# Optimization experiments

Measured on AMD Instinct MI355X. Metric: run time of the kernel, lower is better.

## Reference

```python
import jax, jax.numpy as jnp
import numpy as np

# ---- static IOBES label set: 'O' + {B,I,E,S}-T{t} for 12 entity types -> 49 labels ----
N_TYPES = 12
LABEL_NAMES = ['O'] + [f'{p}-T{t}' for t in range(N_TYPES) for p in ('B', 'I', 'E', 'S')]
L = len(LABEL_NAMES)  # 49

def _build_allow():
    # ALLOW[prev, nxt] True iff transition prev->nxt is NOT masked by mask_logits
    A = np.zeros((L, L), dtype=bool)
    for i, pname in enumerate(LABEL_NAMES):
        if pname[0] in 'OES':
            for j, nname in enumerate(LABEL_NAMES):
                A[i, j] = nname[0] in 'OBS'
        else:  # B-tag or I-tag: only I-tag / E-tag allowed
            tag = pname.split('-')[-1]
            for j, nname in enumerate(LABEL_NAMES):
                A[i, j] = nname in (f'I-{tag}', f'E-{tag}')
    return A

ALLOW = jnp.asarray(_build_allow())
NEG = -1e12

B, S, H, E = 64, 512, 1024, 128


def setup_inputs() -> dict:
    key = jax.random.key(0)
    ks = jax.random.split(key, 8)
    scale = 0.02
    return {
        'word_embeddings': jax.random.normal(ks[0], (B, S, H), dtype=jnp.float32),
        'label_ids': jax.random.randint(ks[1], (B, S), 0, L, dtype=jnp.int32),
        'emb_table': jax.random.normal(ks[2], (L, E), dtype=jnp.float32) * scale,
        'w_ih': jax.random.normal(ks[3], (3 * H, E + H), dtype=jnp.float32) * scale,
        'w_hh': jax.random.normal(ks[4], (3 * H, H), dtype=jnp.float32) * scale,
        'b_ih': jnp.zeros((3 * H,), dtype=jnp.float32),
        'b_hh': jnp.zeros((3 * H,), dtype=jnp.float32),
        'w_out': jax.random.normal(ks[5], (L, H), dtype=jnp.float32) * scale,
        'b_out': jnp.zeros((L,), dtype=jnp.float32),
    }


def reference(word_embeddings, label_ids, emb_table, w_ih, w_hh, b_ih, b_hh, w_out, b_out):
    Bn, Sn, Hn = word_embeddings.shape
    # teacher-forced previous labels, shifted right with 'O' (index 0) start token
    start = jnp.zeros((Bn, 1), dtype=label_ids.dtype)
    prev_ids = jnp.concatenate([start, label_ids], axis=1)[:, :-1]  # [B,S]
    # per-step GRU input: [prev label embedding ; word embedding]
    x = jnp.concatenate([emb_table[prev_ids], word_embeddings], axis=-1)  # [B,S,E+H]
    # precompute input contributions to all 3 gates for every step
    gx = jnp.einsum('bsi,gi->bsg', x, w_ih) + b_ih  # [B,S,3H], gate order r,z,n (torch)
    h0 = jnp.zeros((Bn, Hn), dtype=word_embeddings.dtype)

    def step(h, gxt):
        gh = h @ w_hh.T + b_hh  # [B,3H]
        r = jax.nn.sigmoid(gxt[:, :Hn] + gh[:, :Hn])
        z = jax.nn.sigmoid(gxt[:, Hn:2 * Hn] + gh[:, Hn:2 * Hn])
        n = jnp.tanh(gxt[:, 2 * Hn:] + r * gh[:, 2 * Hn:])
        h_new = (1.0 - z) * n + z * h
        return h_new, h_new

    _, outs = jax.lax.scan(step, h0, jnp.swapaxes(gx, 0, 1))  # [S,B,H]
    outs = jnp.swapaxes(outs, 0, 1)  # [B,S,H]
    logits = outs @ w_out.T + b_out  # [B,S,L]
    # label-transition masking based on previous label id (static IOBES constraint)
    logits = jnp.where(ALLOW[prev_ids], logits, NEG)
    return logits
```

## Files before the change

### kernel.cpp

```cpp
#include <hip/hip_runtime.h>
#include <cstdint>
#include <cstddef>

#define B_ 64
#define S_ 512
#define H_ 1024
#define E_ 128
#define L_ 49
#define G3_ 3072
#define K_ 1152
#define C_ 64
#define NCH_ 8

typedef short bf16x8 __attribute__((ext_vector_type(8)));
typedef float f32x4 __attribute__((ext_vector_type(4)));
typedef unsigned int u32x2 __attribute__((ext_vector_type(2)));

__device__ __forceinline__ unsigned short f2bf(float f) {
  unsigned int u = __builtin_bit_cast(unsigned int, f);
  return (unsigned short)((u + 0x7FFFu + ((u >> 16) & 1u)) >> 16);
}
__device__ __forceinline__ float bf2f(unsigned short h) {
  unsigned int u = ((unsigned int)h) << 16;
  return __builtin_bit_cast(float, u);
}

#define GLOAD16(dst, a64) asm volatile("global_load_dwordx4 %0, %1, off sc0 sc1" : "=v"(dst) : "v"(a64))
#define GLOAD8(dst, a64)  asm volatile("global_load_dwordx2 %0, %1, off sc0 sc1" : "=v"(dst) : "v"(a64))
#define GSTORE8(a64, v2)  asm volatile("global_store_dwordx2 %0, %1, off sc0 sc1" :: "v"(a64), "v"(v2) : "memory")
#define WAITV(N) asm volatile("s_waitcnt vmcnt(" #N ")")

__global__ __launch_bounds__(256) void init_kernel(float4* __restrict__ p)
{
  const int i = blockIdx.x * 256 + threadIdx.x;
  p[i] = make_float4(0.f, 0.f, 0.f, 0.f);
}

__global__ __launch_bounds__(256) void gx_gemm(
    const float* __restrict__ word, const int* __restrict__ labels,
    const float* __restrict__ emb, const float* __restrict__ w_ih,
    const float* __restrict__ b_ih, float* __restrict__ gxC, int t0)
{
  __shared__ float xs[2][32][72];
  __shared__ float wsm[2][32][136];

  const int bid = blockIdx.x;
  const int Tl = bid / 24;
  const int T  = t0 + Tl;
  const int cb = bid % 24;
  const int tid = threadIdx.x;

  const int xb = tid >> 2, xkq = tid & 3;
  const int pid = (T > 0) ? labels[xb * S_ + T - 1] : 0;
  const float* xsrcA = emb + (size_t)pid * E_;
  const float* xsrcB = word + ((size_t)xb * S_ + T) * H_ - E_;
  const int wc = tid >> 1, wkh = tid & 1;
  const float* wrow = w_ih + (size_t)(cb * 128 + wc) * K_;

  float4 xr0, xr1, wr0, wr1, wr2, wr3;

  auto load_tile = [&](int kt) {
    const int kg = kt * 32;
    const float* xsrc = (kg < E_) ? (xsrcA + kg) : (xsrcB + kg);
    xr0 = *(const float4*)(xsrc + xkq * 8);
    xr1 = *(const float4*)(xsrc + xkq * 8 + 4);
    const float* wsrc = wrow + kg + wkh * 16;
    wr0 = *(const float4*)(wsrc);
    wr1 = *(const float4*)(wsrc + 4);
    wr2 = *(const float4*)(wsrc + 8);
    wr3 = *(const float4*)(wsrc + 12);
  };
  auto store_tile = [&](int bf) {
#pragma unroll
    for (int i = 0; i < 4; ++i) xs[bf][xkq * 8 + i][xb]     = ((const float*)&xr0)[i];
#pragma unroll
    for (int i = 0; i < 4; ++i) xs[bf][xkq * 8 + 4 + i][xb] = ((const float*)&xr1)[i];
#pragma unroll
    for (int i = 0; i < 4; ++i) wsm[bf][wkh * 16 + i][wc]      = ((const float*)&wr0)[i];
#pragma unroll
    for (int i = 0; i < 4; ++i) wsm[bf][wkh * 16 + 4 + i][wc]  = ((const float*)&wr1)[i];
#pragma unroll
    for (int i = 0; i < 4; ++i) wsm[bf][wkh * 16 + 8 + i][wc]  = ((const float*)&wr2)[i];
#pragma unroll
    for (int i = 0; i < 4; ++i) wsm[bf][wkh * 16 + 12 + i][wc] = ((const float*)&wr3)[i];
  };

  const int cg = tid >> 4, bg = tid & 15;
  float acc[8][4];
#pragma unroll
  for (int i = 0; i < 8; ++i)
#pragma unroll
    for (int j = 0; j < 4; ++j) acc[i][j] = 0.f;

  load_tile(0);
  store_tile(0);
  __syncthreads();

  for (int kt = 0; kt < 36; ++kt) {
    const int cur = kt & 1;
    if (kt < 35) load_tile(kt + 1);
#pragma unroll 4
    for (int k = 0; k < 32; ++k) {
      const float4 xv  = *(const float4*)&xs[cur][k][bg * 4];
      const float4 wv0 = *(const float4*)&wsm[cur][k][cg * 8];
      const float4 wv1 = *(const float4*)&wsm[cur][k][cg * 8 + 4];
      const float wv[8] = {wv0.x, wv0.y, wv0.z, wv0.w, wv1.x, wv1.y, wv1.z, wv1.w};
      const float xa[4] = {xv.x, xv.y, xv.z, xv.w};
#pragma unroll
      for (int ci = 0; ci < 8; ++ci)
#pragma unroll
        for (int bi = 0; bi < 4; ++bi)
          acc[ci][bi] = fmaf(wv[ci], xa[bi], acc[ci][bi]);
    }
    if (kt < 35) store_tile(cur ^ 1);
    __syncthreads();
  }

  const size_t obase = ((size_t)Tl * G3_ + (size_t)cb * 128) * 64;
#pragma unroll
  for (int ci = 0; ci < 8; ++ci) {
    const int c = cg * 8 + ci;
    const float bv = b_ih[cb * 128 + c];
    float4 o;
    o.x = acc[ci][0] + bv; o.y = acc[ci][1] + bv;
    o.z = acc[ci][2] + bv; o.w = acc[ci][3] + bv;
    *(float4*)&gxC[obase + (size_t)c * 64 + bg * 4] = o;
  }
}

__global__ __launch_bounds__(256, 1) void scan_kernel(
    const float* __restrict__ gxC, const float* __restrict__ w_hh,
    const float* __restrict__ b_hh,
    char* phiA, char* ploA, char* phiB, char* ploB,
    float* __restrict__ outsC, unsigned* bar, unsigned step0)
{
  const int g = blockIdx.x;
  const int tid = threadIdx.x;
  const int lane = tid & 63;
  const int w = tid >> 6;
  const int m = lane & 15;
  const int gA = lane >> 4;
  const int bl = m;

  bf16x8 whi[32], wlo[32];
  {
    const bool valid = (m < 12);
    const int msafe = valid ? m : 0;
    const float* wr = w_hh + (size_t)((msafe >> 2) * 1024 + 4 * g + (msafe & 3)) * 1024;
#pragma unroll
    for (int ks = 0; ks < 32; ++ks) {
      const int kb = ks * 32 + gA * 8;
      float v[8];
      const float4 a0 = *(const float4*)(wr + kb);
      const float4 a1 = *(const float4*)(wr + kb + 4);
      v[0] = a0.x; v[1] = a0.y; v[2] = a0.z; v[3] = a0.w;
      v[4] = a1.x; v[5] = a1.y; v[6] = a1.z; v[7] = a1.w;
#pragma unroll
      for (int i = 0; i < 8; ++i) {
        const float f = valid ? v[i] : 0.f;
        const unsigned short hh = f2bf(f);
        const unsigned short hl = f2bf(f - bf2f(hh));
        whi[ks][i] = (short)hh;
        wlo[ks][i] = (short)hl;
      }
    }
  }

  const int ksj = g >> 3;
  const int gf  = (g >> 1) & 3;
  const unsigned gbyte =
      ((unsigned)((ksj * 4 + w) * 64 + gf * 16 + bl)) * 16u + 8u * (g & 1);
  float bh_r[4], bh_z[4], bh_n[4], hold[4];
#pragma unroll
  for (int jj = 0; jj < 4; ++jj) {
    bh_r[jj] = b_hh[4 * g + jj];
    bh_z[jj] = b_hh[1024 + 4 * g + jj];
    bh_n[jj] = b_hh[2048 + 4 * g + jj];
  }
  {
    u32x2 dh, dl;
    GLOAD8(dh, (uint64_t)(uintptr_t)(phiA + gbyte));
    GLOAD8(dl, (uint64_t)(uintptr_t)(ploA + gbyte));
    WAITV(0);
    __builtin_amdgcn_sched_barrier(0);
#pragma unroll
    for (int jj = 0; jj < 4; ++jj) {
      const unsigned short hh = (unsigned short)((dh[jj >> 1] >> ((jj & 1) * 16)) & 0xFFFFu);
      const unsigned short hl = (unsigned short)((dl[jj >> 1] >> ((jj & 1) * 16)) & 0xFFFFu);
      hold[jj] = bf2f(hh) + bf2f(hl);
    }
  }

  char* curHi = phiA; char* curLo = ploA;
  char* nxtHi = phiB; char* nxtLo = ploB;

  for (int s = 0; s < C_; ++s) {
    float gr[4], gz[4], gn[4];
    {
      const float* gp = gxC + (size_t)s * (G3_ * 64) + 16 * w + bl;
#pragma unroll
      for (int jj = 0; jj < 4; ++jj) {
        gr[jj] = gp[(0 * 1024 + 4 * g + jj) * 64];
        gz[jj] = gp[(1 * 1024 + 4 * g + jj) * 64];
        gn[jj] = gp[(2 * 1024 + 4 * g + jj) * 64];
      }
    }

    const uint64_t bHi = (uint64_t)(uintptr_t)curHi + (unsigned)((w << 10) + (lane << 4));
    const uint64_t bLo = (uint64_t)(uintptr_t)curLo + (unsigned)((w << 10) + (lane << 4));
    bf16x8 bh[2][4], blo[2][4];
    f32x4 acc[6];
#pragma unroll
    for (int c = 0; c < 6; ++c) acc[c] = (f32x4){0.f, 0.f, 0.f, 0.f};

#pragma unroll
    for (int q = 0; q < 4; ++q) {
      GLOAD16(bh[0][q],  bHi + (unsigned)((0 * 4 + q) * 4096));
      GLOAD16(blo[0][q], bLo + (unsigned)((0 * 4 + q) * 4096));
    }
#pragma unroll
    for (int q = 0; q < 4; ++q) {
      GLOAD16(bh[1][q],  bHi + (unsigned)((1 * 4 + q) * 4096));
      GLOAD16(blo[1][q], bLo + (unsigned)((1 * 4 + q) * 4096));
    }

#pragma unroll
    for (int grp = 0; grp < 8; ++grp) {
      if (grp < 7) { WAITV(8); } else { WAITV(0); }
      __builtin_amdgcn_sched_barrier(0);
      const int buf = grp & 1;
#pragma unroll
      for (int q = 0; q < 4; ++q) {
        const int ks = grp * 4 + q;
        const int p = (ks & 1) * 3;
        acc[p + 0] = __builtin_amdgcn_mfma_f32_16x16x32_bf16(whi[ks], bh[buf][q],  acc[p + 0], 0, 0, 0);
        acc[p + 1] = __builtin_amdgcn_mfma_f32_16x16x32_bf16(whi[ks], blo[buf][q], acc[p + 1], 0, 0, 0);
        acc[p + 2] = __builtin_amdgcn_mfma_f32_16x16x32_bf16(wlo[ks], bh[buf][q],  acc[p + 2], 0, 0, 0);
      }
      if (grp + 2 < 8) {
#pragma unroll
        for (int q = 0; q < 4; ++q) {
          GLOAD16(bh[buf][q],  bHi + (unsigned)(((grp + 2) * 4 + q) * 4096));
          GLOAD16(blo[buf][q], bLo + (unsigned)(((grp + 2) * 4 + q) * 4096));
        }
      }
    }

    f32x4 P = (acc[0] + acc[3]) + (acc[1] + acc[4]) + (acc[2] + acc[5]);

    float zs[4], ns[4];
#pragma unroll
    for (int jj = 0; jj < 4; ++jj) {
      zs[jj] = __shfl(P[jj], bl + 16);
      ns[jj] = __shfl(P[jj], bl + 32);
    }

    if (lane < 16) {
      const int b = 16 * w + bl;
      unsigned short hhi[4], hlo[4];
#pragma unroll
      for (int jj = 0; jj < 4; ++jj) {
        const float r = 1.f / (1.f + expf(-(gr[jj] + P[jj] + bh_r[jj])));
        const float z = 1.f / (1.f + expf(-(gz[jj] + zs[jj] + bh_z[jj])));
        const float n = tanhf(gn[jj] + r * (ns[jj] + bh_n[jj]));
        const float hnew = (1.f - z) * n + z * hold[jj];
        hold[jj] = hnew;
        outsC[((size_t)s << 16) + (size_t)((4 * g + jj) << 6) + b] = hnew;
        hhi[jj] = f2bf(hnew);
        hlo[jj] = f2bf(hnew - bf2f(hhi[jj]));
      }
      u32x2 vh, vl;
      vh[0] = (unsigned)hhi[0] | ((unsigned)hhi[1] << 16);
      vh[1] = (unsigned)hhi[2] | ((unsigned)hhi[3] << 16);
      vl[0] = (unsigned)hlo[0] | ((unsigned)hlo[1] << 16);
      vl[1] = (unsigned)hlo[2] | ((unsigned)hlo[3] << 16);
      GSTORE8((uint64_t)(uintptr_t)(nxtHi + gbyte), vh);
      GSTORE8((uint64_t)(uintptr_t)(nxtLo + gbyte), vl);
    }

    __syncthreads();
    if (tid == 0) {
      asm volatile("s_waitcnt vmcnt(0)" ::: "memory");
      const unsigned tgt = step0 + (unsigned)s + 1u;
      const unsigned old =
          __hip_atomic_fetch_add(bar, 1u, __ATOMIC_RELAXED, __HIP_MEMORY_SCOPE_AGENT);
      if (old == 255u) {
        __hip_atomic_store(bar, 0u, __ATOMIC_RELAXED, __HIP_MEMORY_SCOPE_AGENT);
        asm volatile("s_waitcnt vmcnt(0)" ::: "memory");
        __hip_atomic_store(bar + 544, tgt, __ATOMIC_RELAXED, __HIP_MEMORY_SCOPE_AGENT);
      } else {
        while (__hip_atomic_load(bar + 544, __ATOMIC_RELAXED, __HIP_MEMORY_SCOPE_AGENT) < tgt)
          __builtin_amdgcn_s_sleep(1);
      }
    }
    __syncthreads();

    char* t1 = curHi; curHi = nxtHi; nxtHi = t1;
    char* t2 = curLo; curLo = nxtLo; nxtLo = t2;
  }
}

__global__ __launch_bounds__(256) void logits_kernel(
    const float* __restrict__ outsC, const int* __restrict__ labels,
    const float* __restrict__ w_out, const float* __restrict__ b_out,
    float* __restrict__ out, int t0)
{
  __shared__ float hs[128 * 64];
  __shared__ float wso[49 * 128];
  const int tl = blockIdx.x;
  const int t  = t0 + tl;
  const int tid = threadIdx.x;
  const int b = tid & 63, lq = tid >> 6;
  const int l0 = lq * 13;
  const int nl = (lq == 3) ? 10 : 13;

  float acc[13];
#pragma unroll
  for (int i = 0; i < 13; ++i) acc[i] = 0.f;

  for (int kc = 0; kc < 8; ++kc) {
    __syncthreads();
#pragma unroll
    for (int i = 0; i < 8; ++i) {
      const int flat = (i << 10) + (tid << 2);
      *(float4*)&hs[flat] = *(const float4*)&outsC[((size_t)tl << 16) + (kc << 13) + flat];
    }
    for (int idx = tid; idx < 1568; idx += 256) {
      const int l = idx >> 5, k4 = idx & 31;
      *(float4*)&wso[l * 128 + (k4 << 2)] =
          *(const float4*)&w_out[(size_t)l * 1024 + (kc << 7) + (k4 << 2)];
    }
    __syncthreads();
    for (int k = 0; k < 128; k += 4) {
      const float h0 = hs[((k + 0) << 6) + b];
      const float h1 = hs[((k + 1) << 6) + b];
      const float h2 = hs[((k + 2) << 6) + b];
      const float h3 = hs[((k + 3) << 6) + b];
#pragma unroll
      for (int li = 0; li < 13; ++li) {
        if (li < nl) {
          const float4 wv = *(const float4*)&wso[(l0 + li) * 128 + k];
          acc[li] = fmaf(wv.w, h3, fmaf(wv.z, h2, fmaf(wv.y, h1, fmaf(wv.x, h0, acc[li]))));
        }
      }
    }
  }

  const int pid = (t > 0) ? labels[b * S_ + t - 1] : 0;
  bool prevOES;
  int ptype = 0;
  if (pid == 0) { prevOES = true; }
  else {
    const int pp = (pid - 1) & 3;
    prevOES = (pp >= 2);
    ptype = (pid - 1) >> 2;
  }
#pragma unroll
  for (int li = 0; li < 13; ++li) {
    if (li < nl) {
      const int l = l0 + li;
      bool ok;
      if (prevOES) {
        ok = (l == 0) || (((l - 1) & 3) == 0) || (((l - 1) & 3) == 3);
      } else {
        ok = (l > 0) && (((l - 1) >> 2) == ptype) &&
             ((((l - 1) & 3) == 1) || (((l - 1) & 3) == 2));
      }
      out[(((size_t)b << 9) + t) * 49 + l] = ok ? (acc[li] + b_out[l]) : -1e12f;
    }
  }
}

extern "C" void kernel_launch(void* const* d_in, const int* in_sizes, int n_in,
                              void* d_out, int out_size, void* d_ws, size_t ws_size,
                              hipStream_t stream)
{
  const float* word   = (const float*)d_in[0];
  const int*   labels = (const int*)d_in[1];
  const float* emb    = (const float*)d_in[2];
  const float* w_ih   = (const float*)d_in[3];
  const float* w_hh   = (const float*)d_in[4];
  const float* b_ih   = (const float*)d_in[5];
  const float* b_hh   = (const float*)d_in[6];
  const float* w_out  = (const float*)d_in[7];
  const float* b_out  = (const float*)d_in[8];
  float* out = (float*)d_out;

  char* ws = (char*)d_ws;
  float*    gxC   = (float*)ws;
  float*    outsC = (float*)(ws + 50331648ull);
  char*     phiA  = ws + 67108864ull;
  char*     ploA  = ws + 67239936ull;
  char*     phiB  = ws + 67371008ull;
  char*     ploB  = ws + 67502080ull;
  unsigned* bar   = (unsigned*)(ws + 67633152ull);

  init_kernel<<<dim3(129), dim3(256), 0, stream>>>((float4*)phiA);

  for (int ch = 0; ch < NCH_; ++ch) {
    const int t0 = ch * C_;
    gx_gemm<<<dim3(C_ * 24), dim3(256), 0, stream>>>(word, labels, emb, w_ih, b_ih,
                                                     gxC, t0);
    scan_kernel<<<dim3(256), dim3(256), 0, stream>>>(gxC, w_hh, b_hh,
                                                     phiA, ploA, phiB, ploB,
                                                     outsC, bar, (unsigned)t0);
    logits_kernel<<<dim3(C_), dim3(256), 0, stream>>>(outsC, labels, w_out, b_out,
                                                      out, t0);
  }
}
```

Measured before the change: 8.332 ms.

## Replace FP32 input-gate GEMM with split-bf16 MFMA and halve chunk size

```diff
diff --git a/kernel.cpp b/kernel.cpp
--- a/kernel.cpp
+++ b/kernel.cpp
@@ -9,8 +9,8 @@
 #define L_ 49
 #define G3_ 3072
 #define K_ 1152
-#define C_ 64
-#define NCH_ 8
+#define C_ 32
+#define NCH_ 16
 
 typedef short bf16x8 __attribute__((ext_vector_type(8)));
 typedef float f32x4 __attribute__((ext_vector_type(4)));
@@ -36,95 +36,123 @@
   p[i] = make_float4(0.f, 0.f, 0.f, 0.f);
 }
 
-__global__ __launch_bounds__(256) void gx_gemm(
+__global__ __launch_bounds__(256) void prep_w(
+    const float* __restrict__ w_ih, short* __restrict__ Wh, short* __restrict__ Wl)
+{
+  const int idx = blockIdx.x * 256 + threadIdx.x;
+  const int m = idx & 127;
+  const int slot = idx >> 7;
+  const int kg = slot & 3;
+  const int cks = slot >> 2;
+  const int ks = cks % 36, ct = cks / 36;
+  const float* src = w_ih + (size_t)(ct * 128 + m) * K_ + (ks * 32 + kg * 8);
+  bf16x8 h, l;
+#pragma unroll
+  for (int i = 0; i < 8; ++i) {
+    const float f = src[i];
+    const unsigned short hh = f2bf(f);
+    h[i] = (short)hh;
+    l[i] = (short)f2bf(f - bf2f(hh));
+  }
+  *(bf16x8*)(Wh + (size_t)idx * 8) = h;
+  *(bf16x8*)(Wl + (size_t)idx * 8) = l;
+}
+
+__global__ __launch_bounds__(256) void prep_x(
     const float* __restrict__ word, const int* __restrict__ labels,
-    const float* __restrict__ emb, const float* __restrict__ w_ih,
-    const float* __restrict__ b_ih, float* __restrict__ gxC, int t0)
-{
-  __shared__ float xs[2][32][72];
-  __shared__ float wsm[2][32][136];
-
-  const int bid = blockIdx.x;
-  const int Tl = bid / 24;
-  const int T  = t0 + Tl;
-  const int cb = bid % 24;
+    const float* __restrict__ emb, short* __restrict__ Xh, short* __restrict__ Xl,
+    int t0)
+{
+  const int idx = blockIdx.x * 256 + threadIdx.x;
+  const int n = idx & 2047;
+  const int s8 = idx >> 11;
+  const int tl = n >> 6, b = n & 63;
+  const int t = t0 + tl;
+  const int k0 = s8 * 8;
+  const float* src;
+  if (k0 < E_) {
+    const int pid = (t > 0) ? labels[b * S_ + t - 1] : 0;
+    src = emb + (size_t)pid * E_ + k0;
+  } else {
+    src = word + ((size_t)b * S_ + t) * H_ + (k0 - E_);
+  }
+  bf16x8 h, l;
+#pragma unroll
+  for (int i = 0; i < 8; ++i) {
+    const float f = src[i];
+    const unsigned short hh = f2bf(f);
+    h[i] = (short)hh;
+    l[i] = (short)f2bf(f - bf2f(hh));
+  }
+  *(bf16x8*)(Xh + (size_t)idx * 8) = h;
+  *(bf16x8*)(Xl + (size_t)idx * 8) = l;
+}
+
+__global__ __launch_bounds__(256, 2) void gx_mfma(
+    const short* __restrict__ Wh, const short* __restrict__ Wl,
+    const short* __restrict__ Xh, const short* __restrict__ Xl,
+    const float* __restrict__ b_ih, float* __restrict__ gxC)
+{
   const int tid = threadIdx.x;
-
-  const int xb = tid >> 2, xkq = tid & 3;
-  const int pid = (T > 0) ? labels[xb * S_ + T - 1] : 0;
-  const float* xsrcA = emb + (size_t)pid * E_;
-  const float* xsrcB = word + ((size_t)xb * S_ + T) * H_ - E_;
-  const int wc = tid >> 1, wkh = tid & 1;
-  const float* wrow = w_ih + (size_t)(cb * 128 + wc) * K_;
-
-  float4 xr0, xr1, wr0, wr1, wr2, wr3;
-
-  auto load_tile = [&](int kt) {
-    const int kg = kt * 32;
-    const float* xsrc = (kg < E_) ? (xsrcA + kg) : (xsrcB + kg);
-    xr0 = *(const float4*)(xsrc + xkq * 8);
-    xr1 = *(const float4*)(xsrc + xkq * 8 + 4);
-    const float* wsrc = wrow + kg + wkh * 16;
-    wr0 = *(const float4*)(wsrc);
-    wr1 = *(const float4*)(wsrc + 4);
-    wr2 = *(const float4*)(wsrc + 8);
-    wr3 = *(const float4*)(wsrc + 12);
-  };
-  auto store_tile = [&](int bf) {
-#pragma unroll
-    for (int i = 0; i < 4; ++i) xs[bf][xkq * 8 + i][xb]     = ((const float*)&xr0)[i];
-#pragma unroll
-    for (int i = 0; i < 4; ++i) xs[bf][xkq * 8 + 4 + i][xb] = ((const float*)&xr1)[i];
-#pragma unroll
-    for (int i = 0; i < 4; ++i) wsm[bf][wkh * 16 + i][wc]      = ((const float*)&wr0)[i];
-#pragma unroll
-    for (int i = 0; i < 4; ++i) wsm[bf][wkh * 16 + 4 + i][wc]  = ((const float*)&wr1)[i];
-#pragma unroll
-    for (int i = 0; i < 4; ++i) wsm[bf][wkh * 16 + 8 + i][wc]  = ((const float*)&wr2)[i];
-#pragma unroll
-    for (int i = 0; i < 4; ++i) wsm[bf][wkh * 16 + 12 + i][wc] = ((const float*)&wr3)[i];
-  };
-
-  const int cg = tid >> 4, bg = tid & 15;
-  float acc[8][4];
-#pragma unroll
-  for (int i = 0; i < 8; ++i)
-#pragma unroll
-    for (int j = 0; j < 4; ++j) acc[i][j] = 0.f;
-
-  load_tile(0);
-  store_tile(0);
-  __syncthreads();
-
-  for (int kt = 0; kt < 36; ++kt) {
-    const int cur = kt & 1;
-    if (kt < 35) load_tile(kt + 1);
-#pragma unroll 4
-    for (int k = 0; k < 32; ++k) {
-      const float4 xv  = *(const float4*)&xs[cur][k][bg * 4];
-      const float4 wv0 = *(const float4*)&wsm[cur][k][cg * 8];
-      const float4 wv1 = *(const float4*)&wsm[cur][k][cg * 8 + 4];
-      const float wv[8] = {wv0.x, wv0.y, wv0.z, wv0.w, wv1.x, wv1.y, wv1.z, wv1.w};
-      const float xa[4] = {xv.x, xv.y, xv.z, xv.w};
-#pragma unroll
-      for (int ci = 0; ci < 8; ++ci)
-#pragma unroll
-        for (int bi = 0; bi < 4; ++bi)
-          acc[ci][bi] = fmaf(wv[ci], xa[bi], acc[ci][bi]);
-    }
-    if (kt < 35) store_tile(cur ^ 1);
-    __syncthreads();
-  }
-
-  const size_t obase = ((size_t)Tl * G3_ + (size_t)cb * 128) * 64;
-#pragma unroll
-  for (int ci = 0; ci < 8; ++ci) {
-    const int c = cg * 8 + ci;
-    const float bv = b_ih[cb * 128 + c];
-    float4 o;
-    o.x = acc[ci][0] + bv; o.y = acc[ci][1] + bv;
-    o.z = acc[ci][2] + bv; o.w = acc[ci][3] + bv;
-    *(float4*)&gxC[obase + (size_t)c * 64 + bg * 4] = o;
+  const int nt = blockIdx.x & 15, ct = blockIdx.x >> 4;
+  const int lane = tid & 63, w = tid >> 6;
+  const int wm = w & 1, wn = w >> 1;
+  const int lo16 = lane & 15, hi4 = lane >> 4;
+
+  const size_t abase = ((size_t)(ct * 36) * 512 + (size_t)hi4 * 128 + wm * 64 + lo16) * 8;
+  const size_t bbase = ((size_t)hi4 * 2048 + nt * 128 + wn * 64 + lo16) * 8;
+
+  bf16x8 ah[2][4], al[2][4], xh[2][4], xl[2][4];
+  f32x4 acc[4][4];
+#pragma unroll
+  for (int a = 0; a < 4; ++a)
+#pragma unroll
+    for (int bq = 0; bq < 4; ++bq) acc[a][bq] = (f32x4){0.f, 0.f, 0.f, 0.f};
+
+#pragma unroll
+  for (int f = 0; f < 4; ++f) {
+    ah[0][f] = *(const bf16x8*)(Wh + abase + (size_t)f * 128);
+    al[0][f] = *(const bf16x8*)(Wl + abase + (size_t)f * 128);
+    xh[0][f] = *(const bf16x8*)(Xh + bbase + (size_t)f * 128);
+    xl[0][f] = *(const bf16x8*)(Xl + bbase + (size_t)f * 128);
+  }
+
+#pragma unroll
+  for (int ks = 0; ks < 36; ++ks) {
+    const int cur = ks & 1;
+    if (ks < 35) {
+      const size_t a1 = abase + (size_t)(ks + 1) * 4096;
+      const size_t b1 = bbase + (size_t)(ks + 1) * 65536;
+#pragma unroll
+      for (int f = 0; f < 4; ++f) {
+        ah[cur ^ 1][f] = *(const bf16x8*)(Wh + a1 + (size_t)f * 128);
+        al[cur ^ 1][f] = *(const bf16x8*)(Wl + a1 + (size_t)f * 128);
+        xh[cur ^ 1][f] = *(const bf16x8*)(Xh + b1 + (size_t)f * 128);
+        xl[cur ^ 1][f] = *(const bf16x8*)(Xl + b1 + (size_t)f * 128);
+      }
+    }
+#pragma unroll
+    for (int mf = 0; mf < 4; ++mf)
+#pragma unroll
+      for (int nf = 0; nf < 4; ++nf) {
+        acc[mf][nf] = __builtin_amdgcn_mfma_f32_16x16x32_bf16(ah[cur][mf], xh[cur][nf], acc[mf][nf], 0, 0, 0);
+        acc[mf][nf] = __builtin_amdgcn_mfma_f32_16x16x32_bf16(ah[cur][mf], xl[cur][nf], acc[mf][nf], 0, 0, 0);
+        acc[mf][nf] = __builtin_amdgcn_mfma_f32_16x16x32_bf16(al[cur][mf], xh[cur][nf], acc[mf][nf], 0, 0, 0);
+      }
+  }
+
+  const int tl = nt * 2 + wn;
+  float* outb = gxC + (size_t)tl * (G3_ * 64);
+#pragma unroll
+  for (int mf = 0; mf < 4; ++mf) {
+    const int c0 = ct * 128 + wm * 64 + mf * 16 + hi4 * 4;
+#pragma unroll
+    for (int r = 0; r < 4; ++r) {
+      const float bv = b_ih[c0 + r];
+#pragma unroll
+      for (int nf = 0; nf < 4; ++nf)
+        outb[(size_t)(c0 + r) * 64 + nf * 16 + lo16] = acc[mf][nf][r] + bv;
+    }
   }
 }
 
@@ -386,21 +414,28 @@
   const float* b_out  = (const float*)d_in[8];
   float* out = (float*)d_out;
 
+  if (ws_size < 49287168ull) return;
+
   char* ws = (char*)d_ws;
   float*    gxC   = (float*)ws;
-  float*    outsC = (float*)(ws + 50331648ull);
-  char*     phiA  = ws + 67108864ull;
-  char*     ploA  = ws + 67239936ull;
-  char*     phiB  = ws + 67371008ull;
-  char*     ploB  = ws + 67502080ull;
-  unsigned* bar   = (unsigned*)(ws + 67633152ull);
+  short*    Xh    = (short*)(ws + 25165824ull);
+  short*    Xl    = (short*)(ws + 29884416ull);
+  float*    outsC = (float*)(ws + 25165824ull);
+  char*     phiA  = ws + 34603008ull;
+  char*     ploA  = ws + 34734080ull;
+  char*     phiB  = ws + 34865152ull;
+  char*     ploB  = ws + 34996224ull;
+  unsigned* bar   = (unsigned*)(ws + 35127296ull);
+  short*    Wh    = (short*)(ws + 35131392ull);
+  short*    Wl    = (short*)(ws + 42209280ull);
 
   init_kernel<<<dim3(129), dim3(256), 0, stream>>>((float4*)phiA);
+  prep_w<<<dim3(1728), dim3(256), 0, stream>>>(w_ih, Wh, Wl);
 
   for (int ch = 0; ch < NCH_; ++ch) {
     const int t0 = ch * C_;
-    gx_gemm<<<dim3(C_ * 24), dim3(256), 0, stream>>>(word, labels, emb, w_ih, b_ih,
-                                                     gxC, t0);
+    prep_x<<<dim3(1152), dim3(256), 0, stream>>>(word, labels, emb, Xh, Xl, t0);
+    gx_mfma<<<dim3(384), dim3(256), 0, stream>>>(Wh, Wl, Xh, Xl, b_ih, gxC);
     scan_kernel<<<dim3(256), dim3(256), 0, stream>>>(gxC, w_hh, b_hh,
                                                      phiA, ploA, phiB, ploB,
                                                      outsC, bar, (unsigned)t0);
```

Result: slower. 8.509 ms (+2.1%).
